# Kernel tuning notes

Hardware: AMD Instinct MI355X
Metric: run time of the kernel (lower is better)

## Reference

```python
import jax, jax.numpy as jnp
import numpy as np

B, S, D = 2, 2048, 2048
HQ, HKV, HD = 16, 4, 128
G = HQ // HKV  # repeat factor for GQA
SCALE = HD ** -0.5


def setup_inputs() -> dict:
    key = jax.random.key(0)
    k = jax.random.split(key, 6)
    return {
        "x": jax.random.normal(k[0], (B, S, D), jnp.float32),
        "Wq": jax.random.normal(k[1], (D, HQ * HD), jnp.float32) * 0.02,
        "Wk": jax.random.normal(k[2], (D, HKV * HD), jnp.float32) * 0.02,
        "Wv": jax.random.normal(k[3], (D, HKV * HD), jnp.float32) * 0.02,
        "Wo": jax.random.normal(k[4], (HQ * HD, D), jnp.float32) * 0.02,
        "bo": jnp.zeros((D,), jnp.float32),
    }


def reference(x, Wq, Wk, Wv, Wo, bo):
    b, s, _ = x.shape
    # projections (Linear, no bias for q/k/v)
    q = (x @ Wq).reshape(b, s, HQ, HD).transpose(0, 2, 1, 3)    # [b,Hq,s,hd]
    k = (x @ Wk).reshape(b, s, HKV, HD).transpose(0, 2, 1, 3)   # [b,Hkv,s,hd]
    v = (x @ Wv).reshape(b, s, HKV, HD).transpose(0, 2, 1, 3)
    # group query heads per kv head: repeat_interleave(k, G, dim=1) means
    # q head h attends to kv head h // G -> reshape q to [b,Hkv,G,s,hd]
    qg = q.reshape(b, HKV, G, s, HD)
    sim = jnp.einsum("bkgid,bkjd->bkgij", qg, k) * SCALE        # [b,Hkv,G,s,s]
    attn = jax.nn.softmax(sim, axis=-1)                          # dropout p=0 (eval)
    out = jnp.einsum("bkgij,bkjd->bkgid", attn, v)               # [b,Hkv,G,s,hd]
    out = out.reshape(b, HQ, s, HD).transpose(0, 2, 1, 3).reshape(b, s, HQ * HD)
    return out @ Wo + bo
```

## Files before the change

### kernel.cpp

```cpp
#include <hip/hip_runtime.h>
#include <hip/hip_bf16.h>
#include <stdint.h>

typedef unsigned short u16;
typedef __attribute__((ext_vector_type(8))) short short8;
typedef __attribute__((ext_vector_type(4))) short short4v;
typedef __attribute__((ext_vector_type(4))) float f32x4;

#define B_N   2
#define S_LEN 2048
#define D_MOD 2048
#define N_HQ  16
#define N_HKV 4
#define N_HD  128

__device__ __forceinline__ u16 f2b(float f) {
  union { float f; uint32_t u; } v; v.f = f;
  uint32_t r = v.u + 0x7fffu + ((v.u >> 16) & 1u);
  return (u16)(r >> 16);
}

__device__ __forceinline__ void gload_lds16(const void* g, void* l) {
  __builtin_amdgcn_global_load_lds((__attribute__((address_space(1))) void*)g,
                                   (__attribute__((address_space(3))) void*)l,
                                   16, 0, 0);
}

__global__ void k_cvt(const float* __restrict__ in, u16* __restrict__ out, int n) {
  int i = (blockIdx.x * blockDim.x + threadIdx.x) * 8;
  if (i >= n) return;
  float4 a = *(const float4*)(in + i);
  float4 b = *(const float4*)(in + i + 4);
  short8 o;
  o[0] = (short)f2b(a.x); o[1] = (short)f2b(a.y);
  o[2] = (short)f2b(a.z); o[3] = (short)f2b(a.w);
  o[4] = (short)f2b(b.x); o[5] = (short)f2b(b.y);
  o[6] = (short)f2b(b.z); o[7] = (short)f2b(b.w);
  *(short8*)(out + i) = o;
}

__global__ void k_cvt_t_all(const float* __restrict__ Wq, const float* __restrict__ Wk,
                            const float* __restrict__ Wv, const float* __restrict__ Wo,
                            u16* __restrict__ Wqt, u16* __restrict__ Wkt,
                            u16* __restrict__ Wvt, u16* __restrict__ Wot) {
  __shared__ float tile[32][33];
  const int bx = blockIdx.x;
  const float* W; u16* Wt; int N, n0;
  if (bx < 64)      { W = Wq; Wt = Wqt; N = 2048; n0 = bx * 32; }
  else if (bx < 80) { W = Wk; Wt = Wkt; N = 512;  n0 = (bx - 64) * 32; }
  else if (bx < 96) { W = Wv; Wt = Wvt; N = 512;  n0 = (bx - 80) * 32; }
  else              { W = Wo; Wt = Wot; N = 2048; n0 = (bx - 96) * 32; }
  const int k0 = blockIdx.y * 32;
  int tx = threadIdx.x, ty = threadIdx.y;
#pragma unroll
  for (int i = 0; i < 4; i++) {
    int r = ty + i * 8;
    tile[r][tx] = W[(size_t)(k0 + r) * N + n0 + tx];
  }
  __syncthreads();
#pragma unroll
  for (int i = 0; i < 4; i++) {
    int r = ty + i * 8;
    Wt[(size_t)(n0 + r) * 2048 + k0 + tx] = f2b(tile[tx][r]);
  }
}

__global__ __launch_bounds__(256, 2) void k_gemm_qkv(
    const u16* __restrict__ A,
    const u16* __restrict__ Wqt, const u16* __restrict__ Wkt, const u16* __restrict__ Wvt,
    u16* __restrict__ Qout, u16* __restrict__ Kout, u16* __restrict__ Vt,
    float qscale)
{
  __shared__ __attribute__((aligned(16))) u16 lA[128 * 64];
  __shared__ __attribute__((aligned(16))) u16 lB[128 * 64];
  const int K = D_MOD;
  const int tid = threadIdx.x;
  const int lane = tid & 63, w = tid >> 6;
  const int wr = w >> 1, wc = w & 1;
  const int lin = blockIdx.y * 24 + blockIdx.x;
  const int swz = (lin & 7) * 96 + (lin >> 3);
  const int bx = swz % 24;
  const int kind = bx < 16 ? 0 : (bx < 20 ? 1 : 2);
  const int bcol = (kind == 0 ? bx : (bx & 3)) * 128;
  const u16* Bt = kind == 0 ? Wqt : (kind == 1 ? Wkt : Wvt);
  const int brow = (swz / 24) * 128;
  const int lrow = lane >> 3;
  const int lkc = (lane & 7) * 8;
  const int l15 = lane & 15, lg = lane >> 4;

  f32x4 acc[4][4] = {};

  for (int kt = 0; kt < K; kt += 64) {
#pragma unroll
    for (int i = 0; i < 4; i++) {
      int row = (w * 4 + i) * 8 + lrow;
      gload_lds16(A + (size_t)(brow + row) * K + kt + lkc, &lA[(w * 4 + i) * 512]);
      gload_lds16(Bt + (size_t)(bcol + row) * K + kt + lkc, &lB[(w * 4 + i) * 512]);
    }
    __syncthreads();
#pragma unroll
    for (int kk = 0; kk < 2; kk++) {
      short8 af[4], bf[4];
#pragma unroll
      for (int m = 0; m < 4; m++)
        af[m] = *(const short8*)&lA[(wr * 64 + m * 16 + l15) * 64 + kk * 32 + lg * 8];
#pragma unroll
      for (int n = 0; n < 4; n++)
        bf[n] = *(const short8*)&lB[(wc * 64 + n * 16 + l15) * 64 + kk * 32 + lg * 8];
#pragma unroll
      for (int m = 0; m < 4; m++)
#pragma unroll
        for (int n = 0; n < 4; n++)
          acc[m][n] = __builtin_amdgcn_mfma_f32_16x16x32_bf16(af[m], bf[n], acc[m][n], 0, 0, 0);
    }
    __syncthreads();
  }

#pragma unroll
  for (int m = 0; m < 4; m++) {
#pragma unroll
    for (int n = 0; n < 4; n++) {
#pragma unroll
      for (int r = 0; r < 4; r++) {
        float v = acc[m][n][r];
        int row = brow + wr * 64 + m * 16 + lg * 4 + r;
        int col = bcol + wc * 64 + n * 16 + l15;
        if (kind == 0) {
          Qout[(size_t)row * (N_HQ * N_HD) + col] = f2b(v * qscale);
        } else if (kind == 1) {
          Kout[(size_t)row * (N_HKV * N_HD) + col] = f2b(v);
        } else {
          int bb = row >> 11, s = row & 2047;
          int sp = (s & ~63) | (((s & 15) << 2) | ((s >> 4) & 3));
          int hkv = col >> 7, d = col & 127;
          Vt[((size_t)((bb * N_HKV + hkv) * N_HD + d)) * S_LEN + sp] = f2b(v);
        }
      }
    }
  }
}

__global__ __launch_bounds__(256, 2) void k_gemm_o(
    const u16* __restrict__ A, const u16* __restrict__ Bt,
    float* __restrict__ Cout, const float* __restrict__ bias,
    int M, int N, int K)
{
  __shared__ __attribute__((aligned(16))) u16 lA[128 * 64];
  __shared__ __attribute__((aligned(16))) u16 lB[128 * 64];
  const int tid = threadIdx.x;
  const int lane = tid & 63, w = tid >> 6;
  const int wr = w >> 1, wc = w & 1;
  const int lin = blockIdx.y * 16 + blockIdx.x;
  const int swz = (lin & 7) * 64 + (lin >> 3);
  const int brow = (swz / 16) * 128, bcol = (swz % 16) * 128;
  const int lrow = lane >> 3;
  const int lkc = (lane & 7) * 8;
  const int l15 = lane & 15, lg = lane >> 4;

  f32x4 acc[4][4] = {};

  for (int kt = 0; kt < K; kt += 64) {
#pragma unroll
    for (int i = 0; i < 4; i++) {
      int row = (w * 4 + i) * 8 + lrow;
      gload_lds16(A + (size_t)(brow + row) * K + kt + lkc, &lA[(w * 4 + i) * 512]);
      gload_lds16(Bt + (size_t)(bcol + row) * K + kt + lkc, &lB[(w * 4 + i) * 512]);
    }
    __syncthreads();
#pragma unroll
    for (int kk = 0; kk < 2; kk++) {
      short8 af[4], bf[4];
#pragma unroll
      for (int m = 0; m < 4; m++)
        af[m] = *(const short8*)&lA[(wr * 64 + m * 16 + l15) * 64 + kk * 32 + lg * 8];
#pragma unroll
      for (int n = 0; n < 4; n++)
        bf[n] = *(const short8*)&lB[(wc * 64 + n * 16 + l15) * 64 + kk * 32 + lg * 8];
#pragma unroll
      for (int m = 0; m < 4; m++)
#pragma unroll
        for (int n = 0; n < 4; n++)
          acc[m][n] = __builtin_amdgcn_mfma_f32_16x16x32_bf16(af[m], bf[n], acc[m][n], 0, 0, 0);
    }
    __syncthreads();
  }

#pragma unroll
  for (int m = 0; m < 4; m++) {
#pragma unroll
    for (int n = 0; n < 4; n++) {
#pragma unroll
      for (int r = 0; r < 4; r++) {
        int row = brow + wr * 64 + m * 16 + lg * 4 + r;
        int col = bcol + wc * 64 + n * 16 + l15;
        Cout[(size_t)row * N + col] = acc[m][n][r] + bias[col];
      }
    }
  }
}

__global__ __launch_bounds__(256, 2) void k_attn(
    const u16* __restrict__ Q,
    const u16* __restrict__ Kb,
    const u16* __restrict__ Vt,
    u16* __restrict__ O)
{
  __shared__ __attribute__((aligned(16))) u16 lK[64 * 128];
  __shared__ __attribute__((aligned(16))) u16 lV[128 * 64];
  __shared__ __attribute__((aligned(16))) u16 p_lds[4][32][76];
  const int lane = threadIdx.x & 63, w = threadIdx.x >> 6;
  const int lin = blockIdx.z * 256 + blockIdx.y * 16 + blockIdx.x;
  const int swz = (lin & 7) * 64 + (lin >> 3);
  const int qt = swz & 15, h = (swz >> 4) & 15, b = swz >> 8;
  const int hkv = h >> 2;
  const int qbase = qt * 128 + w * 32;
  const int l15 = lane & 15, lg = lane >> 4;
  const int l7 = lane & 7, l3 = lane >> 3;

  const u16* kbp = Kb + (size_t)(b * S_LEN) * (N_HKV * N_HD) + hkv * N_HD;
  const u16* vbp = Vt + (size_t)((b * N_HKV + hkv) * N_HD) * S_LEN;

  short8 qf[2][4];
#pragma unroll
  for (int s = 0; s < 2; s++) {
    const u16* qptr = Q + (size_t)(b * S_LEN + qbase + s * 16 + l15) * (N_HQ * N_HD) + h * N_HD + lg * 8;
#pragma unroll
    for (int kk = 0; kk < 4; kk++) qf[s][kk] = *(const short8*)(qptr + kk * 32);
  }

  f32x4 acc_o[2][8] = {};
  f32x4 acc_ls[2] = {};
  short8 vone;
#pragma unroll
  for (int j = 0; j < 8; j++) vone[j] = (short)0x3F80;

  short8 kreg[4], vreg[4];
  const int kchm = l15 ^ ((w * 4 + lg) & 7);
  const int vchm = l7 ^ l3;

#define LOADREGS(ktv) do {                                                           \
    _Pragma("unroll")                                                                \
    for (int i = 0; i < 4; i++) {                                                    \
      kreg[i] = *(const short8*)(kbp + (size_t)((ktv) + i * 16 + w * 4 + lg) * (N_HKV * N_HD) + kchm * 8); \
      vreg[i] = *(const short8*)(vbp + (size_t)(i * 32 + w * 8 + l3) * S_LEN + (ktv) + vchm * 8);          \
    } } while (0)

#define WRITEREGS() do {                                                             \
    _Pragma("unroll")                                                                \
    for (int i = 0; i < 4; i++) {                                                    \
      *(short8*)&lK[(i * 16 + w * 4) * 128 + lane * 8] = kreg[i];                    \
      *(short8*)&lV[(i * 32 + w * 8) * 64 + lane * 8] = vreg[i];                     \
    } } while (0)

  LOADREGS(0);
  WRITEREGS();
  __syncthreads();

  const int NT = S_LEN / 64;
  for (int it = 0; it < NT; ++it) {
    if (it + 1 < NT) LOADREGS((it + 1) * 64);

    f32x4 sc[2][4] = {};
#pragma unroll
    for (int nf = 0; nf < 4; nf++) {
      int krow = nf * 16 + l15;
      const u16* kro = &lK[krow * 128];
#pragma unroll
      for (int kk = 0; kk < 4; kk++) {
        short8 kf = *(const short8*)&kro[(((kk * 4 + lg) ^ (krow & 7)) * 8)];
#pragma unroll
        for (int s = 0; s < 2; s++)
          sc[s][nf] = __builtin_amdgcn_mfma_f32_16x16x32_bf16(qf[s][kk], kf, sc[s][nf], 0, 0, 0);
      }
    }

#pragma unroll
    for (int s = 0; s < 2; s++)
#pragma unroll
      for (int r = 0; r < 4; r++) {
        short4v pq;
#pragma unroll
        for (int nf = 0; nf < 4; nf++)
          pq[nf] = (short)f2b(__builtin_amdgcn_exp2f(sc[s][nf][r]));
        *(short4v*)&p_lds[w][s * 16 + lg * 4 + r][l15 * 4] = pq;
      }

    asm volatile("s_waitcnt lgkmcnt(0)" ::: "memory");
    __builtin_amdgcn_sched_barrier(0);

    short8 pf[2][2];
#pragma unroll
    for (int s = 0; s < 2; s++)
#pragma unroll
      for (int p2 = 0; p2 < 2; p2++)
        pf[s][p2] = *(const short8*)&p_lds[w][s * 16 + l15][p2 * 32 + lg * 8];

#pragma unroll
    for (int s = 0; s < 2; s++)
#pragma unroll
      for (int p2 = 0; p2 < 2; p2++)
        acc_ls[s] = __builtin_amdgcn_mfma_f32_16x16x32_bf16(pf[s][p2], vone, acc_ls[s], 0, 0, 0);

#pragma unroll
    for (int nc = 0; nc < 8; nc++) {
      int vrow = nc * 16 + l15;
      const u16* vro = &lV[vrow * 64];
#pragma unroll
      for (int p2 = 0; p2 < 2; p2++) {
        short8 vf = *(const short8*)&vro[(((p2 * 4 + lg) ^ (vrow & 7)) * 8)];
#pragma unroll
        for (int s = 0; s < 2; s++)
          acc_o[s][nc] = __builtin_amdgcn_mfma_f32_16x16x32_bf16(pf[s][p2], vf, acc_o[s][nc], 0, 0, 0);
      }
    }

    __syncthreads();
    if (it + 1 < NT) WRITEREGS();
    __syncthreads();
  }
#undef LOADREGS
#undef WRITEREGS

#pragma unroll
  for (int s = 0; s < 2; s++)
#pragma unroll
    for (int r = 0; r < 4; r++) {
      float inv = 1.f / acc_ls[s][r];
      size_t row = (size_t)(b * S_LEN + qbase + s * 16 + lg * 4 + r);
#pragma unroll
      for (int nc = 0; nc < 8; nc++)
        O[row * (N_HQ * N_HD) + h * N_HD + nc * 16 + l15] = f2b(acc_o[s][nc][r] * inv);
    }
}

extern "C" void kernel_launch(void* const* d_in, const int* in_sizes, int n_in,
                              void* d_out, int out_size, void* d_ws, size_t ws_size,
                              hipStream_t stream) {
  const float* x  = (const float*)d_in[0];
  const float* Wq = (const float*)d_in[1];
  const float* Wk = (const float*)d_in[2];
  const float* Wv = (const float*)d_in[3];
  const float* Wo = (const float*)d_in[4];
  const float* bo = (const float*)d_in[5];
  float* out = (float*)d_out;

  char* ws = (char*)d_ws;
  u16* x_bf = (u16*)(ws + 0);
  u16* Wqt  = (u16*)(ws + 16777216);
  u16* Wkt  = (u16*)(ws + 25165824);
  u16* Wvt  = (u16*)(ws + 27262976);
  u16* Wot  = (u16*)(ws + 29360128);
  u16* Qb   = (u16*)(ws + 37748736);
  u16* Kbuf = (u16*)(ws + 54525952);
  u16* Vt   = (u16*)(ws + 58720256);
  u16* AO   = (u16*)(ws + 0);

  const int n_x = B_N * S_LEN * D_MOD;
  k_cvt<<<n_x / (8 * 256), 256, 0, stream>>>(x, x_bf, n_x);

  k_cvt_t_all<<<dim3(160, 64), dim3(32, 8), 0, stream>>>(
      Wq, Wk, Wv, Wo, Wqt, Wkt, Wvt, Wot);

  const int M = B_N * S_LEN;
  const float qscale = 1.4426950408889634f / sqrtf((float)N_HD);

  k_gemm_qkv<<<dim3(24, M / 128), 256, 0, stream>>>(
      x_bf, Wqt, Wkt, Wvt, Qb, Kbuf, Vt, qscale);

  k_attn<<<dim3(S_LEN / 128, N_HQ, B_N), 256, 0, stream>>>(Qb, Kbuf, Vt, AO);

  k_gemm_o<<<dim3(D_MOD / 128, M / 128), 256, 0, stream>>>(
      AO, Wot, out, bo, M, D_MOD, N_HQ * N_HD);
}
```

Measured before the change: 218.0 us.

## Double-buffer attention K/V via direct global-to-LDS loads and keep P in registers

The attention kernel now double-buffers K and V tiles in LDS, filling them with global_load_lds straight into shared memory. This replaces the register round-trip and removes one barrier per iteration. The QK^T MFMA operands are swapped and K rows are permuted so the score fragment already matches the PV A-operand layout. That lets P be built in registers instead of going through an LDS staging buffer, and the V pre-permutation in the QKV GEMM epilogue is dropped. Separately, the QKV GEMM launch bound is raised to 3 blocks per CU, which may force register spills in exchange for occupancy.

Result: faster. 210.2 us (-3.6%).

```diff
diff --git a/kernel.cpp b/kernel.cpp
--- a/kernel.cpp
+++ b/kernel.cpp
@@ -4,7 +4,6 @@
 
 typedef unsigned short u16;
 typedef __attribute__((ext_vector_type(8))) short short8;
-typedef __attribute__((ext_vector_type(4))) short short4v;
 typedef __attribute__((ext_vector_type(4))) float f32x4;
 
 #define B_N   2
@@ -65,7 +64,7 @@
   }
 }
 
-__global__ __launch_bounds__(256, 2) void k_gemm_qkv(
+__global__ __launch_bounds__(256, 3) void k_gemm_qkv(
     const u16* __restrict__ A,
     const u16* __restrict__ Wqt, const u16* __restrict__ Wkt, const u16* __restrict__ Wvt,
     u16* __restrict__ Qout, u16* __restrict__ Kout, u16* __restrict__ Vt,
@@ -131,9 +130,8 @@
           Kout[(size_t)row * (N_HKV * N_HD) + col] = f2b(v);
         } else {
           int bb = row >> 11, s = row & 2047;
-          int sp = (s & ~63) | (((s & 15) << 2) | ((s >> 4) & 3));
           int hkv = col >> 7, d = col & 127;
-          Vt[((size_t)((bb * N_HKV + hkv) * N_HD + d)) * S_LEN + sp] = f2b(v);
+          Vt[((size_t)((bb * N_HKV + hkv) * N_HD + d)) * S_LEN + s] = f2b(v);
         }
       }
     }
@@ -205,9 +203,8 @@
     const u16* __restrict__ Vt,
     u16* __restrict__ O)
 {
-  __shared__ __attribute__((aligned(16))) u16 lK[64 * 128];
-  __shared__ __attribute__((aligned(16))) u16 lV[128 * 64];
-  __shared__ __attribute__((aligned(16))) u16 p_lds[4][32][76];
+  __shared__ __attribute__((aligned(16))) u16 lK[2][64 * 128];
+  __shared__ __attribute__((aligned(16))) u16 lV[2][128 * 64];
   const int lane = threadIdx.x & 63, w = threadIdx.x >> 6;
   const int lin = blockIdx.z * 256 + blockIdx.y * 16 + blockIdx.x;
   const int swz = (lin & 7) * 64 + (lin >> 3);
@@ -234,66 +231,49 @@
 #pragma unroll
   for (int j = 0; j < 8; j++) vone[j] = (short)0x3F80;
 
-  short8 kreg[4], vreg[4];
-  const int kchm = l15 ^ ((w * 4 + lg) & 7);
-  const int vchm = l7 ^ l3;
-
-#define LOADREGS(ktv) do {                                                           \
+#define STAGE(bufi, ktv) do {                                                        \
     _Pragma("unroll")                                                                \
     for (int i = 0; i < 4; i++) {                                                    \
-      kreg[i] = *(const short8*)(kbp + (size_t)((ktv) + i * 16 + w * 4 + lg) * (N_HKV * N_HD) + kchm * 8); \
-      vreg[i] = *(const short8*)(vbp + (size_t)(i * 32 + w * 8 + l3) * S_LEN + (ktv) + vchm * 8);          \
+      int kr = i * 16 + w * 4 + lg;                                                  \
+      int sx = (kr & 3) ^ (((kr >> 3) & 3) << 1);                                    \
+      gload_lds16(kbp + (size_t)((ktv) + kr) * (N_HKV * N_HD) + ((l15 ^ sx)) * 8,    \
+                  &lK[bufi][(i * 16 + w * 4) * 128]);                                \
+      int vr = i * 32 + w * 8 + l3;                                                  \
+      gload_lds16(vbp + (size_t)vr * S_LEN + (ktv) + ((l7 ^ (vr & 7))) * 8,          \
+                  &lV[bufi][(i * 32 + w * 8) * 64]);                                 \
     } } while (0)
 
-#define WRITEREGS() do {                                                             \
-    _Pragma("unroll")                                                                \
-    for (int i = 0; i < 4; i++) {                                                    \
-      *(short8*)&lK[(i * 16 + w * 4) * 128 + lane * 8] = kreg[i];                    \
-      *(short8*)&lV[(i * 32 + w * 8) * 64 + lane * 8] = vreg[i];                     \
-    } } while (0)
-
-  LOADREGS(0);
-  WRITEREGS();
+  STAGE(0, 0);
   __syncthreads();
 
+  const int sxr = (l15 & 3) ^ (((l15 >> 2) & 3) << 1);
   const int NT = S_LEN / 64;
+  int buf = 0;
   for (int it = 0; it < NT; ++it) {
-    if (it + 1 < NT) LOADREGS((it + 1) * 64);
+    if (it + 1 < NT) STAGE(buf ^ 1, (it + 1) * 64);
 
     f32x4 sc[2][4] = {};
 #pragma unroll
     for (int nf = 0; nf < 4; nf++) {
-      int krow = nf * 16 + l15;
-      const u16* kro = &lK[krow * 128];
+      int krow = (nf >> 1) * 32 + ((l15 >> 2) * 8) + ((nf & 1) * 4) + (l15 & 3);
+      const u16* kro = &lK[buf][krow * 128];
 #pragma unroll
       for (int kk = 0; kk < 4; kk++) {
-        short8 kf = *(const short8*)&kro[(((kk * 4 + lg) ^ (krow & 7)) * 8)];
+        short8 kf = *(const short8*)&kro[(((kk * 4 + lg) ^ sxr) * 8)];
 #pragma unroll
         for (int s = 0; s < 2; s++)
-          sc[s][nf] = __builtin_amdgcn_mfma_f32_16x16x32_bf16(qf[s][kk], kf, sc[s][nf], 0, 0, 0);
+          sc[s][nf] = __builtin_amdgcn_mfma_f32_16x16x32_bf16(kf, qf[s][kk], sc[s][nf], 0, 0, 0);
       }
     }
 
+    short8 pf[2][2];
 #pragma unroll
     for (int s = 0; s < 2; s++)
 #pragma unroll
-      for (int r = 0; r < 4; r++) {
-        short4v pq;
-#pragma unroll
-        for (int nf = 0; nf < 4; nf++)
-          pq[nf] = (short)f2b(__builtin_amdgcn_exp2f(sc[s][nf][r]));
-        *(short4v*)&p_lds[w][s * 16 + lg * 4 + r][l15 * 4] = pq;
-      }
-
-    asm volatile("s_waitcnt lgkmcnt(0)" ::: "memory");
-    __builtin_amdgcn_sched_barrier(0);
-
-    short8 pf[2][2];
-#pragma unroll
-    for (int s = 0; s < 2; s++)
-#pragma unroll
       for (int p2 = 0; p2 < 2; p2++)
-        pf[s][p2] = *(const short8*)&p_lds[w][s * 16 + l15][p2 * 32 + lg * 8];
+#pragma unroll
+        for (int e = 0; e < 8; e++)
+          pf[s][p2][e] = (short)f2b(__builtin_amdgcn_exp2f(sc[s][p2 * 2 + (e >> 2)][e & 3]));
 
 #pragma unroll
     for (int s = 0; s < 2; s++)
@@ -304,7 +284,7 @@
 #pragma unroll
     for (int nc = 0; nc < 8; nc++) {
       int vrow = nc * 16 + l15;
-      const u16* vro = &lV[vrow * 64];
+      const u16* vro = &lV[buf][vrow * 64];
 #pragma unroll
       for (int p2 = 0; p2 < 2; p2++) {
         short8 vf = *(const short8*)&vro[(((p2 * 4 + lg) ^ (vrow & 7)) * 8)];
@@ -315,11 +295,9 @@
     }
 
     __syncthreads();
-    if (it + 1 < NT) WRITEREGS();
-    __syncthreads();
-  }
-#undef LOADREGS
-#undef WRITEREGS
+    buf ^= 1;
+  }
+#undef STAGE
 
 #pragma unroll
   for (int s = 0; s < 2; s++)
```
